# Optimization experiments

Measured on AMD Instinct MI355X. Metric: run time of the kernel, lower is better.

Reference implementation:

```python
import jax, jax.numpy as jnp
import numpy as np

DIM = 768
HEADS = 12
CLS = 20
HIDDEN = 4 * DIM
EPS = 1e-5


def layernorm(x, g, b):
    m = jnp.mean(x, axis=-1, keepdims=True)
    v = jnp.var(x, axis=-1, keepdims=True)
    return (x - m) * jax.lax.rsqrt(v + EPS) * g + b


def setup_inputs() -> dict:
    key = jax.random.key(0)
    ks = jax.random.split(key, 8)
    s = 0.02
    return {
        "x": jax.random.normal(ks[0], (16, 596, DIM), dtype=jnp.float32),
        "qkv_w": jax.random.normal(ks[1], (3 * DIM, DIM), dtype=jnp.float32) * s,
        "qkv_b": jnp.zeros((3 * DIM,), jnp.float32),
        "proj_w": jax.random.normal(ks[2], (DIM, DIM), dtype=jnp.float32) * s,
        "proj_b": jnp.zeros((DIM,), jnp.float32),
        "ln1_g": jnp.ones((DIM,), jnp.float32),
        "ln1_b": jnp.zeros((DIM,), jnp.float32),
        "ln2_g": jnp.ones((DIM,), jnp.float32),
        "ln2_b": jnp.zeros((DIM,), jnp.float32),
        "fc1_w": jax.random.normal(ks[3], (HIDDEN, DIM), dtype=jnp.float32) * s,
        "fc1_b": jnp.zeros((HIDDEN,), jnp.float32),
        "fc2_w": jax.random.normal(ks[4], (DIM, HIDDEN), dtype=jnp.float32) * s,
        "fc2_b": jnp.zeros((DIM,), jnp.float32),
    }


def attention(x, qkv_w, qkv_b, proj_w, proj_b):
    B, N, C = x.shape
    hd = C // HEADS
    scale = hd ** -0.5
    qkv = x @ qkv_w.T + qkv_b  # [B,N,3C]
    qkv = qkv.reshape(B, N, 3, HEADS, hd).transpose(2, 0, 3, 1, 4)
    q, k, v = qkv[0], qkv[1], qkv[2]  # [B,h,N,hd]
    attn = jnp.einsum("bhqd,bhkd->bhqk", q, k) * scale  # [B,h,N,N]
    # split softmax: first CLS key-columns normalized among themselves,
    # remaining patch columns normalized among themselves.
    attn_cls = jax.nn.softmax(attn[..., :CLS], axis=-1)
    attn_pat = jax.nn.softmax(attn[..., CLS:], axis=-1)
    attn = jnp.concatenate([attn_cls, attn_pat], axis=-1)
    weights = attn
    o = jnp.einsum("bhqk,bhkd->bhqd", attn, v)
    o = o.transpose(0, 2, 1, 3).reshape(B, N, C)
    o = o @ proj_w.T + proj_b
    return o, weights


def reference(x, qkv_w, qkv_b, proj_w, proj_b, ln1_g, ln1_b, ln2_g, ln2_b,
              fc1_w, fc1_b, fc2_w, fc2_b):
    o, weights = attention(layernorm(x, ln1_g, ln1_b), qkv_w, qkv_b, proj_w, proj_b)
    x = x + o
    h = layernorm(x, ln2_g, ln2_b)
    h = jax.nn.gelu(h @ fc1_w.T + fc1_b, approximate=False)
    h = h @ fc2_w.T + fc2_b
    x = x + h
    return x, weights
```

## Files before the change

kernel.cpp:

```cpp
#include <hip/hip_runtime.h>
#include <math.h>

constexpr int DIMC   = 768;
constexpr int NHEADS = 12;
constexpr int HD     = 64;
constexpr int NCLS   = 20;
constexpr int HID    = 3072;
constexpr int NBATCH = 16;
constexpr int NSEQ   = 596;
constexpr int NT     = NBATCH * NSEQ;
constexpr int C3     = 3 * DIMC;
constexpr int MH     = NT / 2;
#define LN_EPS 1e-5f

typedef __attribute__((ext_vector_type(8))) short short8;
typedef __attribute__((ext_vector_type(4))) float f32x4;

__device__ __forceinline__ unsigned short bf16_rn(float f) {
    unsigned u = __float_as_uint(f);
    u += 0x7fffu + ((u >> 16) & 1u);
    return (unsigned short)(u >> 16);
}
__device__ __forceinline__ float bf16_tof(unsigned short h) {
    return __uint_as_float(((unsigned)h) << 16);
}

__device__ __forceinline__ float gelu_f(float v) {
    return 0.5f * v * (1.0f + erff(v * 0.70710678118654752f));
}

typedef __attribute__((address_space(1))) const unsigned int gu32;
typedef __attribute__((address_space(3))) unsigned int lu32;
#define GLOAD16(gp, lp) __builtin_amdgcn_global_load_lds((gu32*)(gp), (lu32*)(lp), 16, 0, 0)

__global__ __launch_bounds__(256) void split_kernel(const float* __restrict__ in,
                                                    unsigned short* __restrict__ hi,
                                                    unsigned short* __restrict__ lo,
                                                    int n4) {
    int i = blockIdx.x * 256 + threadIdx.x;
    const int stp = gridDim.x * 256;
    for (; i < n4; i += stp) {
        const float4 v = ((const float4*)in)[i];
        ushort4 h, l;
        h.x = bf16_rn(v.x); l.x = bf16_rn(v.x - bf16_tof(h.x));
        h.y = bf16_rn(v.y); l.y = bf16_rn(v.y - bf16_tof(h.y));
        h.z = bf16_rn(v.z); l.z = bf16_rn(v.z - bf16_tof(h.z));
        h.w = bf16_rn(v.w); l.w = bf16_rn(v.w - bf16_tof(h.w));
        ((ushort4*)hi)[i] = h;
        ((ushort4*)lo)[i] = l;
    }
}

__global__ __launch_bounds__(256) void ln_kernel(const float* __restrict__ x,
                                                 const float* __restrict__ g,
                                                 const float* __restrict__ b,
                                                 unsigned short* __restrict__ yh,
                                                 unsigned short* __restrict__ yl) {
    const int row = blockIdx.x;
    const float* xr = x + (size_t)row * DIMC;
    const int t = threadIdx.x;
    float v0 = xr[t];
    float v1 = xr[t + 256];
    float v2 = xr[t + 512];
    float s  = v0 + v1 + v2;
    float ss = v0 * v0 + v1 * v1 + v2 * v2;
#pragma unroll
    for (int m = 1; m < 64; m <<= 1) {
        s  += __shfl_xor(s, m);
        ss += __shfl_xor(ss, m);
    }
    __shared__ float ls[4], lss[4];
    const int wid = t >> 6;
    if ((t & 63) == 0) { ls[wid] = s; lss[wid] = ss; }
    __syncthreads();
    s  = ls[0] + ls[1] + ls[2] + ls[3];
    ss = lss[0] + lss[1] + lss[2] + lss[3];
    const float mean = s * (1.0f / DIMC);
    const float var  = ss * (1.0f / DIMC) - mean * mean;
    const float rstd = rsqrtf(var + LN_EPS);
    const size_t base = (size_t)row * DIMC;
#pragma unroll
    for (int e = 0; e < 3; e++) {
        const int c = t + e * 256;
        const float v = (e == 0) ? v0 : (e == 1) ? v1 : v2;
        const float y = (v - mean) * rstd * g[c] + b[c];
        const unsigned short h = bf16_rn(y);
        yh[base + c] = h;
        yl[base + c] = bf16_rn(y - bf16_tof(h));
    }
}

template <int EPI>
__global__ __launch_bounds__(256) void mgemm_kernel(
    const unsigned short* __restrict__ Ah, const unsigned short* __restrict__ Al,
    const unsigned short* __restrict__ Wh, const unsigned short* __restrict__ Wl,
    const float* __restrict__ bias, const float* __restrict__ res,
    float* __restrict__ Out, unsigned short* __restrict__ OutH,
    unsigned short* __restrict__ OutL, int M, int N, int K)
{
    __shared__ unsigned short sAh[128 * 64], sAl[128 * 64];
    __shared__ unsigned short sWh[128 * 64], sWl[128 * 64];

    const int tid  = threadIdx.x;
    const int lane = tid & 63, wid = tid >> 6;
    const int m0 = blockIdx.y * 128, n0 = blockIdx.x * 128;
    const int wr = wid >> 1, wc = wid & 1;

    const int sr = lane >> 3;
    const int sg = (lane & 7) ^ sr;
    size_t goffA[4], goffW[4];
    int ldsoff[4];
#pragma unroll
    for (int t = 0; t < 4; t++) {
        const int r = wid * 32 + t * 8 + sr;
        goffA[t] = (size_t)(m0 + r) * K + sg * 8;
        goffW[t] = (size_t)(n0 + r) * K + sg * 8;
        ldsoff[t] = (wid * 4 + t) * 512;
    }

    const int fr = lane & 15, fe = lane >> 4;
    int offA[2][4], offW[2][4];
#pragma unroll
    for (int k32 = 0; k32 < 2; k32++)
#pragma unroll
        for (int i = 0; i < 4; i++) {
            const int cs = ((k32 * 4 + fe) ^ (fr & 7)) * 8;
            offA[k32][i] = (wr * 64 + i * 16 + fr) * 64 + cs;
            offW[k32][i] = (wc * 64 + i * 16 + fr) * 64 + cs;
        }

    f32x4 acc[4][4];
#pragma unroll
    for (int i = 0; i < 4; i++)
#pragma unroll
        for (int j = 0; j < 4; j++) acc[i][j] = {0.f, 0.f, 0.f, 0.f};

#pragma unroll
    for (int t = 0; t < 4; t++) {
        GLOAD16(Ah + goffA[t], &sAh[ldsoff[t]]);
        GLOAD16(Al + goffA[t], &sAl[ldsoff[t]]);
        GLOAD16(Wh + goffW[t], &sWh[ldsoff[t]]);
        GLOAD16(Wl + goffW[t], &sWl[ldsoff[t]]);
    }

    for (int kt = 0; kt < K; kt += 64) {
        __syncthreads();
#pragma unroll
        for (int k32 = 0; k32 < 2; k32++) {
            short8 a_h[4], a_l[4], w_h[4], w_l[4];
#pragma unroll
            for (int i = 0; i < 4; i++) {
                a_h[i] = *(const short8*)&sAh[offA[k32][i]];
                a_l[i] = *(const short8*)&sAl[offA[k32][i]];
                w_h[i] = *(const short8*)&sWh[offW[k32][i]];
                w_l[i] = *(const short8*)&sWl[offW[k32][i]];
            }
#pragma unroll
            for (int i = 0; i < 4; i++)
#pragma unroll
                for (int j = 0; j < 4; j++) {
                    acc[i][j] = __builtin_amdgcn_mfma_f32_16x16x32_bf16(a_h[i], w_h[j], acc[i][j], 0, 0, 0);
                    acc[i][j] = __builtin_amdgcn_mfma_f32_16x16x32_bf16(a_l[i], w_h[j], acc[i][j], 0, 0, 0);
                    acc[i][j] = __builtin_amdgcn_mfma_f32_16x16x32_bf16(a_h[i], w_l[j], acc[i][j], 0, 0, 0);
                }
        }
        __syncthreads();
        if (kt + 64 < K) {
            const size_t ka = (size_t)(kt + 64);
#pragma unroll
            for (int t = 0; t < 4; t++) {
                GLOAD16(Ah + goffA[t] + ka, &sAh[ldsoff[t]]);
                GLOAD16(Al + goffA[t] + ka, &sAl[ldsoff[t]]);
                GLOAD16(Wh + goffW[t] + ka, &sWh[ldsoff[t]]);
                GLOAD16(Wl + goffW[t] + ka, &sWl[ldsoff[t]]);
            }
        }
    }

#pragma unroll
    for (int j = 0; j < 4; j++) {
        const int col = n0 + wc * 64 + j * 16 + fr;
        const float bj = bias[col];
#pragma unroll
        for (int i = 0; i < 4; i++) {
            const int row0 = m0 + wr * 64 + i * 16 + fe * 4;
#pragma unroll
            for (int q = 0; q < 4; q++) {
                const int gm = row0 + q;
                if (gm < M) {
                    const size_t idx = (size_t)gm * N + col;
                    float v = acc[i][j][q] + bj;
                    if (EPI == 1) v += res[idx];
                    if (EPI == 2) {
                        v = gelu_f(v);
                        const unsigned short hh = bf16_rn(v);
                        OutH[idx] = hh;
                        OutL[idx] = bf16_rn(v - bf16_tof(hh));
                    } else if (EPI == 3) {
                        const unsigned short hh = bf16_rn(v);
                        OutH[idx] = hh;
                        OutL[idx] = bf16_rn(v - bf16_tof(hh));
                    } else {
                        Out[idx] = v;
                    }
                }
            }
        }
    }
}

__global__ __launch_bounds__(256) void fattn_kernel(
    const unsigned short* __restrict__ gqh, const unsigned short* __restrict__ gql,
    float* __restrict__ wts,
    unsigned short* __restrict__ oh, unsigned short* __restrict__ ol)
{
    __shared__ unsigned short Kh[4096], Kl[4096];
    __shared__ unsigned short Vh[4096], Vl[4096];
    __shared__ float Plds[4][16 * 68];

    const int tid = threadIdx.x;
    const int lane = tid & 63, w = tid >> 6;
    const int fr = lane & 15, fe = lane >> 4;
    const int bh = blockIdx.x;
    const int b = bh / NHEADS, h = bh - b * NHEADS;
    const int q0 = blockIdx.y * 64 + w * 16;
    const size_t tokbase = (size_t)b * NSEQ;
    const size_t hoff = (size_t)h * HD;
    const size_t wbase = (size_t)bh * NSEQ * NSEQ;

    short8 qfh[2], qfl[2];
    {
        const short8 z8 = {0, 0, 0, 0, 0, 0, 0, 0};
        qfh[0] = z8; qfh[1] = z8; qfl[0] = z8; qfl[1] = z8;
        const int qi = q0 + fr;
        if (qi < NSEQ) {
            const size_t base = (tokbase + qi) * C3 + hoff + fe * 8;
            qfh[0] = *(const short8*)(gqh + base);
            qfh[1] = *(const short8*)(gqh + base + 32);
            qfl[0] = *(const short8*)(gql + base);
            qfl[1] = *(const short8*)(gql + base + 32);
        }
    }

    const int srow = lane >> 3;
    const int sc8 = (lane & 7) ^ srow;

    float mc[4], mp[4], lc[4], lp[4];
#pragma unroll
    for (int r = 0; r < 4; r++) { mc[r] = -3e38f; mp[r] = -3e38f; lc[r] = 0.f; lp[r] = 0.f; }

    for (int ch = 0; ch < 10; ch++) {
        __syncthreads();
#pragma unroll
        for (int i = 0; i < 2; i++) {
            const int s = w + i * 4;
            const int key = min(ch * 64 + s * 8 + srow, NSEQ - 1);
            const size_t src = (tokbase + key) * C3 + DIMC + hoff + sc8 * 8;
            GLOAD16(gqh + src, &Kh[s * 512]);
            GLOAD16(gql + src, &Kl[s * 512]);
        }
        __syncthreads();

        f32x4 sc_[4];
#pragma unroll
        for (int t = 0; t < 4; t++) sc_[t] = {0.f, 0.f, 0.f, 0.f};
#pragma unroll
        for (int k32 = 0; k32 < 2; k32++)
#pragma unroll
            for (int t = 0; t < 4; t++) {
                const int pos = (t * 16 + fr) * 64 + ((k32 * 4 + fe) ^ (fr & 7)) * 8;
                const short8 kbh = *(const short8*)&Kh[pos];
                const short8 kbl = *(const short8*)&Kl[pos];
                sc_[t] = __builtin_amdgcn_mfma_f32_16x16x32_bf16(qfh[k32], kbh, sc_[t], 0, 0, 0);
                sc_[t] = __builtin_amdgcn_mfma_f32_16x16x32_bf16(qfl[k32], kbh, sc_[t], 0, 0, 0);
                sc_[t] = __builtin_amdgcn_mfma_f32_16x16x32_bf16(qfh[k32], kbl, sc_[t], 0, 0, 0);
            }

        float sv[4][4];
#pragma unroll
        for (int t = 0; t < 4; t++)
#pragma unroll
            for (int r = 0; r < 4; r++) {
                float v = sc_[t][r] * 0.125f;
                if (ch * 64 + t * 16 + fr >= NSEQ) v = -3e38f;
                sv[t][r] = v;
            }

        if (ch == 0) {
#pragma unroll
            for (int r = 0; r < 4; r++) {
                float xc = -3e38f, xp = -3e38f;
#pragma unroll
                for (int t = 0; t < 4; t++) {
                    const bool cls = (t == 0) || (t == 1 && fr < 4);
                    if (cls) xc = fmaxf(xc, sv[t][r]); else xp = fmaxf(xp, sv[t][r]);
                }
#pragma unroll
                for (int o = 1; o < 16; o <<= 1) {
                    xc = fmaxf(xc, __shfl_xor(xc, o));
                    xp = fmaxf(xp, __shfl_xor(xp, o));
                }
                const float mcn = fmaxf(mc[r], xc), mpn = fmaxf(mp[r], xp);
                float ec = 0.f, ep = 0.f;
#pragma unroll
                for (int t = 0; t < 4; t++) {
                    const bool cls = (t == 0) || (t == 1 && fr < 4);
                    const float e = expf(sv[t][r] - (cls ? mcn : mpn));
                    if (cls) ec += e; else ep += e;
                }
#pragma unroll
                for (int o = 1; o < 16; o <<= 1) {
                    ec += __shfl_xor(ec, o);
                    ep += __shfl_xor(ep, o);
                }
                lc[r] = lc[r] * expf(mc[r] - mcn) + ec;
                lp[r] = lp[r] * expf(mp[r] - mpn) + ep;
                mc[r] = mcn; mp[r] = mpn;
            }
        } else {
#pragma unroll
            for (int r = 0; r < 4; r++) {
                float xp = fmaxf(fmaxf(sv[0][r], sv[1][r]), fmaxf(sv[2][r], sv[3][r]));
#pragma unroll
                for (int o = 1; o < 16; o <<= 1) xp = fmaxf(xp, __shfl_xor(xp, o));
                const float mpn = fmaxf(mp[r], xp);
                float ep = 0.f;
#pragma unroll
                for (int t = 0; t < 4; t++) ep += expf(sv[t][r] - mpn);
#pragma unroll
                for (int o = 1; o < 16; o <<= 1) ep += __shfl_xor(ep, o);
                lp[r] = lp[r] * expf(mp[r] - mpn) + ep;
                mp[r] = mpn;
            }
        }
    }

    float ic[4], ip[4];
#pragma unroll
    for (int r = 0; r < 4; r++) { ic[r] = 1.f / lc[r]; ip[r] = 1.f / lp[r]; }

    f32x4 oacc[4];
#pragma unroll
    for (int dt = 0; dt < 4; dt++) oacc[dt] = {0.f, 0.f, 0.f, 0.f};

    const int dgq = tid & 7;
    const int kp  = tid >> 3;

    for (int ch = 0; ch < 10; ch++) {
        __syncthreads();
#pragma unroll
        for (int i = 0; i < 2; i++) {
            const int s = w + i * 4;
            const int key = min(ch * 64 + s * 8 + srow, NSEQ - 1);
            const size_t src = (tokbase + key) * C3 + DIMC + hoff + sc8 * 8;
            GLOAD16(gqh + src, &Kh[s * 512]);
            GLOAD16(gql + src, &Kl[s * 512]);
        }
        {
            const short8 z8 = {0, 0, 0, 0, 0, 0, 0, 0};
            short8 vah = z8, vAl = z8, vbh = z8, vbl = z8;
            const int keyA = ch * 64 + kp * 2;
            if (keyA < NSEQ) {
                const size_t oA = (tokbase + keyA) * C3 + 2 * DIMC + hoff + dgq * 8;
                vah = *(const short8*)(gqh + oA);
                vAl = *(const short8*)(gql + oA);
            }
            if (keyA + 1 < NSEQ) {
                const size_t oB = (tokbase + keyA + 1) * C3 + 2 * DIMC + hoff + dgq * 8;
                vbh = *(const short8*)(gqh + oB);
                vbl = *(const short8*)(gql + oB);
            }
#pragma unroll
            for (int e = 0; e < 8; e++) {
                const int d = dgq * 8 + e;
                const int col = ((kp >> 2) ^ e ^ dgq) & 7;
                const int wo = d * 32 + col * 4 + (kp & 3);
                ((unsigned int*)Vh)[wo] =
                    (unsigned int)(unsigned short)vah[e] | ((unsigned int)(unsigned short)vbh[e] << 16);
                ((unsigned int*)Vl)[wo] =
                    (unsigned int)(unsigned short)vAl[e] | ((unsigned int)(unsigned short)vbl[e] << 16);
            }
        }
        __syncthreads();

        f32x4 sc_[4];
#pragma unroll
        for (int t = 0; t < 4; t++) sc_[t] = {0.f, 0.f, 0.f, 0.f};
#pragma unroll
        for (int k32 = 0; k32 < 2; k32++)
#pragma unroll
            for (int t = 0; t < 4; t++) {
                const int pos = (t * 16 + fr) * 64 + ((k32 * 4 + fe) ^ (fr & 7)) * 8;
                const short8 kbh = *(const short8*)&Kh[pos];
                const short8 kbl = *(const short8*)&Kl[pos];
                sc_[t] = __builtin_amdgcn_mfma_f32_16x16x32_bf16(qfh[k32], kbh, sc_[t], 0, 0, 0);
                sc_[t] = __builtin_amdgcn_mfma_f32_16x16x32_bf16(qfl[k32], kbh, sc_[t], 0, 0, 0);
                sc_[t] = __builtin_amdgcn_mfma_f32_16x16x32_bf16(qfh[k32], kbl, sc_[t], 0, 0, 0);
            }

#pragma unroll
        for (int t = 0; t < 4; t++)
#pragma unroll
            for (int r = 0; r < 4; r++) {
                const int key = ch * 64 + t * 16 + fr;
                float v = sc_[t][r] * 0.125f;
                if (key >= NSEQ) v = -3e38f;
                const bool cls = key < NCLS;
                const float wv = expf(v - (cls ? mc[r] : mp[r])) * (cls ? ic[r] : ip[r]);
                const int q = q0 + fe * 4 + r;
                if (q < NSEQ && key < NSEQ)
                    wts[wbase + (size_t)q * NSEQ + key] = wv;
                Plds[w][(fe * 4 + r) * 68 + t * 16 + fr] = wv;
            }

#pragma unroll
        for (int kh2 = 0; kh2 < 2; kh2++) {
            float pv[8];
            *(float4*)&pv[0] = *(const float4*)&Plds[w][fr * 68 + kh2 * 32 + fe * 8];
            *(float4*)&pv[4] = *(const float4*)&Plds[w][fr * 68 + kh2 * 32 + fe * 8 + 4];
            short8 ph, pl;
#pragma unroll
            for (int j = 0; j < 8; j++) {
                const unsigned short hh = bf16_rn(pv[j]);
                ph[j] = (short)hh;
                pl[j] = (short)bf16_rn(pv[j] - bf16_tof(hh));
            }
#pragma unroll
            for (int dt = 0; dt < 4; dt++) {
                const int d = dt * 16 + fr;
                const int col = ((kh2 * 4 + fe) ^ (d & 7) ^ ((d >> 3) & 7)) & 7;
                const short8 vfh = *(const short8*)&Vh[d * 64 + col * 8];
                const short8 vfl = *(const short8*)&Vl[d * 64 + col * 8];
                oacc[dt] = __builtin_amdgcn_mfma_f32_16x16x32_bf16(ph, vfh, oacc[dt], 0, 0, 0);
                oacc[dt] = __builtin_amdgcn_mfma_f32_16x16x32_bf16(pl, vfh, oacc[dt], 0, 0, 0);
                oacc[dt] = __builtin_amdgcn_mfma_f32_16x16x32_bf16(ph, vfl, oacc[dt], 0, 0, 0);
            }
        }
    }

#pragma unroll
    for (int dt = 0; dt < 4; dt++)
#pragma unroll
        for (int r = 0; r < 4; r++) {
            const int q = q0 + fe * 4 + r;
            if (q < NSEQ) {
                const size_t idx = (tokbase + q) * DIMC + hoff + dt * 16 + fr;
                const float v = oacc[dt][r];
                const unsigned short hh = bf16_rn(v);
                oh[idx] = hh;
                ol[idx] = bf16_rn(v - bf16_tof(hh));
            }
        }
}

extern "C" void kernel_launch(void* const* d_in, const int* in_sizes, int n_in,
                              void* d_out, int out_size, void* d_ws, size_t ws_size,
                              hipStream_t stream) {
    const float* x      = (const float*)d_in[0];
    const float* qkv_w  = (const float*)d_in[1];
    const float* qkv_b  = (const float*)d_in[2];
    const float* proj_w = (const float*)d_in[3];
    const float* proj_b = (const float*)d_in[4];
    const float* ln1_g  = (const float*)d_in[5];
    const float* ln1_b  = (const float*)d_in[6];
    const float* ln2_g  = (const float*)d_in[7];
    const float* ln2_b  = (const float*)d_in[8];
    const float* fc1_w  = (const float*)d_in[9];
    const float* fc1_b  = (const float*)d_in[10];
    const float* fc2_w  = (const float*)d_in[11];
    const float* fc2_b  = (const float*)d_in[12];

    float* out0 = (float*)d_out;
    float* wts  = out0 + (size_t)NT * DIMC;

    char* ws = (char*)d_ws;
    unsigned short* qkv_h = (unsigned short*)ws;
    unsigned short* qkv_l = qkv_h + (size_t)NT * C3;
    unsigned short* hh_h = (unsigned short*)ws;
    unsigned short* hh_l = hh_h + (size_t)MH * HID;
    char* sReg = ws + (size_t)NT * C3 * 4;
    unsigned short* s_h = (unsigned short*)sReg;
    unsigned short* s_l = s_h + (size_t)NT * DIMC;
    float* x1 = (float*)(sReg + (size_t)NT * DIMC * 4);
    char* wReg = (char*)x1 + (size_t)NT * DIMC * 4;
    unsigned short* qw_h = (unsigned short*)wReg;
    unsigned short* qw_l = qw_h + (size_t)C3 * DIMC;
    unsigned short* pw_h = qw_l + (size_t)C3 * DIMC;
    unsigned short* pw_l = pw_h + (size_t)DIMC * DIMC;
    unsigned short* f1_h = pw_l + (size_t)DIMC * DIMC;
    unsigned short* f1_l = f1_h + (size_t)HID * DIMC;
    unsigned short* f2_h = f1_l + (size_t)HID * DIMC;
    unsigned short* f2_l = f2_h + (size_t)DIMC * HID;

    ln_kernel<<<NT, 256, 0, stream>>>(x, ln1_g, ln1_b, s_h, s_l);
    split_kernel<<<1024, 256, 0, stream>>>(qkv_w, qw_h, qw_l, C3 * DIMC / 4);
    split_kernel<<<576, 256, 0, stream>>>(proj_w, pw_h, pw_l, DIMC * DIMC / 4);
    split_kernel<<<1024, 256, 0, stream>>>(fc1_w, f1_h, f1_l, HID * DIMC / 4);
    split_kernel<<<1024, 256, 0, stream>>>(fc2_w, f2_h, f2_l, DIMC * HID / 4);
    mgemm_kernel<3><<<dim3(C3 / 128, (NT + 127) / 128), 256, 0, stream>>>(
        s_h, s_l, qw_h, qw_l, qkv_b, nullptr, nullptr, qkv_h, qkv_l, NT, C3, DIMC);
    fattn_kernel<<<dim3(NBATCH * NHEADS, 10), 256, 0, stream>>>(qkv_h, qkv_l, wts, s_h, s_l);
    mgemm_kernel<1><<<dim3(DIMC / 128, (NT + 127) / 128), 256, 0, stream>>>(
        s_h, s_l, pw_h, pw_l, proj_b, x, x1, nullptr, nullptr, NT, DIMC, DIMC);
    ln_kernel<<<NT, 256, 0, stream>>>(x1, ln2_g, ln2_b, s_h, s_l);
    for (int hf = 0; hf < 2; hf++) {
        const size_t r0 = (size_t)hf * MH;
        mgemm_kernel<2><<<dim3(HID / 128, (MH + 127) / 128), 256, 0, stream>>>(
            s_h + r0 * DIMC, s_l + r0 * DIMC, f1_h, f1_l, fc1_b, nullptr,
            nullptr, hh_h, hh_l, MH, HID, DIMC);
        mgemm_kernel<1><<<dim3(DIMC / 128, (MH + 127) / 128), 256, 0, stream>>>(
            hh_h, hh_l, f2_h, f2_l, fc2_b, x1 + r0 * DIMC,
            out0 + r0 * DIMC, nullptr, nullptr, MH, DIMC, HID);
    }
}
```

Baseline: 1.245 ms.

## Double-buffer GEMM LDS tiles with packed hi/lo halves and XCD-aware block swizzle

The split-bf16 GEMM now stages K-tiles of 32 with the hi and lo parts packed into one 64-wide LDS row. It double-buffers them so the next tile's global loads are issued before the current tile's MFMAs, which drops one barrier per step. Launches become 1D, and block IDs are remapped so consecutive tiles land on the same XCD, to improve L2 locality. The attention output also skips the lo-residual rounding when the value is exactly representable in bf16. The cost is more loop iterations with smaller K steps and more complex address math.

```diff
diff --git a/kernel.cpp b/kernel.cpp
--- a/kernel.cpp
+++ b/kernel.cpp
@@ -92,89 +92,91 @@
 
 template <int EPI>
 __global__ __launch_bounds__(256) void mgemm_kernel(
-    const unsigned short* __restrict__ Ah, const unsigned short* __restrict__ Al,
-    const unsigned short* __restrict__ Wh, const unsigned short* __restrict__ Wl,
+    const unsigned short* __restrict__ Ah, const unsigned short* __restrict__ Wh,
+    int AloOff, int WloOff,
     const float* __restrict__ bias, const float* __restrict__ res,
     float* __restrict__ Out, unsigned short* __restrict__ OutH,
     unsigned short* __restrict__ OutL, int M, int N, int K)
 {
-    __shared__ unsigned short sAh[128 * 64], sAl[128 * 64];
-    __shared__ unsigned short sWh[128 * 64], sWl[128 * 64];
+    __shared__ unsigned short S[2][2][128 * 64];
 
     const int tid  = threadIdx.x;
     const int lane = tid & 63, wid = tid >> 6;
-    const int m0 = blockIdx.y * 128, n0 = blockIdx.x * 128;
+
+    const int gx = N >> 7;
+    const int nb = gridDim.x;
+    const int qq = nb >> 3, rr = nb & 7;
+    const int xcd = blockIdx.x & 7, bix = blockIdx.x >> 3;
+    const int swz = (xcd < rr ? xcd * (qq + 1) : rr * (qq + 1) + (xcd - rr) * qq) + bix;
+    const int m0 = (swz / gx) * 128, n0 = (swz % gx) * 128;
     const int wr = wid >> 1, wc = wid & 1;
 
-    const int sr = lane >> 3;
-    const int sg = (lane & 7) ^ sr;
     size_t goffA[4], goffW[4];
     int ldsoff[4];
 #pragma unroll
-    for (int t = 0; t < 4; t++) {
-        const int r = wid * 32 + t * 8 + sr;
-        goffA[t] = (size_t)(m0 + r) * K + sg * 8;
-        goffW[t] = (size_t)(n0 + r) * K + sg * 8;
-        ldsoff[t] = (wid * 4 + t) * 512;
+    for (int i = 0; i < 4; i++) {
+        const int rloc = wid * 32 + i * 8 + (lane >> 3);
+        const int u = (lane & 7) ^ (rloc & 7);
+        const int chunk = u & 3, isLo = u >> 2;
+        goffA[i] = (size_t)(m0 + rloc) * K + chunk * 8 + (isLo ? AloOff : 0);
+        goffW[i] = (size_t)(n0 + rloc) * K + chunk * 8 + (isLo ? WloOff : 0);
+        ldsoff[i] = (wid * 4 + i) * 512;
     }
 
     const int fr = lane & 15, fe = lane >> 4;
-    int offA[2][4], offW[2][4];
-#pragma unroll
-    for (int k32 = 0; k32 < 2; k32++)
+    int offAhi[4], offAlo[4], offWhi[4], offWlo[4];
+#pragma unroll
+    for (int i = 0; i < 4; i++) {
+        const int ra = wr * 64 + i * 16 + fr;
+        const int rw = wc * 64 + i * 16 + fr;
+        offAhi[i] = ra * 64 + (fe ^ (ra & 7)) * 8;
+        offAlo[i] = ra * 64 + ((fe ^ 4) ^ (ra & 7)) * 8;
+        offWhi[i] = rw * 64 + (fe ^ (rw & 7)) * 8;
+        offWlo[i] = rw * 64 + ((fe ^ 4) ^ (rw & 7)) * 8;
+    }
+
+    f32x4 acc[4][4];
+#pragma unroll
+    for (int i = 0; i < 4; i++)
+#pragma unroll
+        for (int j = 0; j < 4; j++) acc[i][j] = {0.f, 0.f, 0.f, 0.f};
+
+    const int nt = K >> 5;
+#pragma unroll
+    for (int i = 0; i < 4; i++) {
+        GLOAD16(Ah + goffA[i], &S[0][0][ldsoff[i]]);
+        GLOAD16(Wh + goffW[i], &S[0][1][ldsoff[i]]);
+    }
+
+    for (int t = 0; t < nt; t++) {
+        __syncthreads();
+        if (t + 1 < nt) {
+            const int nxt = (t + 1) & 1;
+            const size_t ka = (size_t)(t + 1) << 5;
+#pragma unroll
+            for (int i = 0; i < 4; i++) {
+                GLOAD16(Ah + goffA[i] + ka, &S[nxt][0][ldsoff[i]]);
+                GLOAD16(Wh + goffW[i] + ka, &S[nxt][1][ldsoff[i]]);
+            }
+        }
+        const unsigned short* sA = &S[t & 1][0][0];
+        const unsigned short* sW = &S[t & 1][1][0];
+        short8 a_h[4], a_l[4], w_h[4], w_l[4];
 #pragma unroll
         for (int i = 0; i < 4; i++) {
-            const int cs = ((k32 * 4 + fe) ^ (fr & 7)) * 8;
-            offA[k32][i] = (wr * 64 + i * 16 + fr) * 64 + cs;
-            offW[k32][i] = (wc * 64 + i * 16 + fr) * 64 + cs;
-        }
-
-    f32x4 acc[4][4];
-#pragma unroll
-    for (int i = 0; i < 4; i++)
-#pragma unroll
-        for (int j = 0; j < 4; j++) acc[i][j] = {0.f, 0.f, 0.f, 0.f};
-
-#pragma unroll
-    for (int t = 0; t < 4; t++) {
-        GLOAD16(Ah + goffA[t], &sAh[ldsoff[t]]);
-        GLOAD16(Al + goffA[t], &sAl[ldsoff[t]]);
-        GLOAD16(Wh + goffW[t], &sWh[ldsoff[t]]);
-        GLOAD16(Wl + goffW[t], &sWl[ldsoff[t]]);
-    }
-
-    for (int kt = 0; kt < K; kt += 64) {
-        __syncthreads();
-#pragma unroll
-        for (int k32 = 0; k32 < 2; k32++) {
-            short8 a_h[4], a_l[4], w_h[4], w_l[4];
-#pragma unroll
-            for (int i = 0; i < 4; i++) {
-                a_h[i] = *(const short8*)&sAh[offA[k32][i]];
-                a_l[i] = *(const short8*)&sAl[offA[k32][i]];
-                w_h[i] = *(const short8*)&sWh[offW[k32][i]];
-                w_l[i] = *(const short8*)&sWl[offW[k32][i]];
-            }
-#pragma unroll
-            for (int i = 0; i < 4; i++)
-#pragma unroll
-                for (int j = 0; j < 4; j++) {
-                    acc[i][j] = __builtin_amdgcn_mfma_f32_16x16x32_bf16(a_h[i], w_h[j], acc[i][j], 0, 0, 0);
-                    acc[i][j] = __builtin_amdgcn_mfma_f32_16x16x32_bf16(a_l[i], w_h[j], acc[i][j], 0, 0, 0);
-                    acc[i][j] = __builtin_amdgcn_mfma_f32_16x16x32_bf16(a_h[i], w_l[j], acc[i][j], 0, 0, 0);
-                }
-        }
-        __syncthreads();
-        if (kt + 64 < K) {
-            const size_t ka = (size_t)(kt + 64);
-#pragma unroll
-            for (int t = 0; t < 4; t++) {
-                GLOAD16(Ah + goffA[t] + ka, &sAh[ldsoff[t]]);
-                GLOAD16(Al + goffA[t] + ka, &sAl[ldsoff[t]]);
-                GLOAD16(Wh + goffW[t] + ka, &sWh[ldsoff[t]]);
-                GLOAD16(Wl + goffW[t] + ka, &sWl[ldsoff[t]]);
-            }
-        }
+            a_h[i] = *(const short8*)&sA[offAhi[i]];
+            a_l[i] = *(const short8*)&sA[offAlo[i]];
+            w_h[i] = *(const short8*)&sW[offWhi[i]];
+            w_l[i] = *(const short8*)&sW[offWlo[i]];
+        }
+#pragma unroll
+        for (int i = 0; i < 4; i++)
+#pragma unroll
+            for (int j = 0; j < 4; j++) {
+                acc[i][j] = __builtin_amdgcn_mfma_f32_16x16x32_bf16(a_h[i], w_h[j], acc[i][j], 0, 0, 0);
+                acc[i][j] = __builtin_amdgcn_mfma_f32_16x16x32_bf16(a_l[i], w_h[j], acc[i][j], 0, 0, 0);
+                acc[i][j] = __builtin_amdgcn_mfma_f32_16x16x32_bf16(a_h[i], w_l[j], acc[i][j], 0, 0, 0);
+            }
     }
 
 #pragma unroll
@@ -448,7 +450,7 @@
                 const float v = oacc[dt][r];
                 const unsigned short hh = bf16_rn(v);
                 oh[idx] = hh;
-                ol[idx] = bf16_rn(v - bf16_tof(hh));
+                ol[idx] = bf16_tof(hh) == v ? 0 : bf16_rn(v - bf16_tof(hh));
             }
         }
 }
@@ -497,19 +499,21 @@
     split_kernel<<<576, 256, 0, stream>>>(proj_w, pw_h, pw_l, DIMC * DIMC / 4);
     split_kernel<<<1024, 256, 0, stream>>>(fc1_w, f1_h, f1_l, HID * DIMC / 4);
     split_kernel<<<1024, 256, 0, stream>>>(fc2_w, f2_h, f2_l, DIMC * HID / 4);
-    mgemm_kernel<3><<<dim3(C3 / 128, (NT + 127) / 128), 256, 0, stream>>>(
-        s_h, s_l, qw_h, qw_l, qkv_b, nullptr, nullptr, qkv_h, qkv_l, NT, C3, DIMC);
+    mgemm_kernel<3><<<(C3 / 128) * ((NT + 127) / 128), 256, 0, stream>>>(
+        s_h, qw_h, NT * DIMC, C3 * DIMC, qkv_b, nullptr,
+        nullptr, qkv_h, qkv_l, NT, C3, DIMC);
     fattn_kernel<<<dim3(NBATCH * NHEADS, 10), 256, 0, stream>>>(qkv_h, qkv_l, wts, s_h, s_l);
-    mgemm_kernel<1><<<dim3(DIMC / 128, (NT + 127) / 128), 256, 0, stream>>>(
-        s_h, s_l, pw_h, pw_l, proj_b, x, x1, nullptr, nullptr, NT, DIMC, DIMC);
+    mgemm_kernel<1><<<(DIMC / 128) * ((NT + 127) / 128), 256, 0, stream>>>(
+        s_h, pw_h, NT * DIMC, DIMC * DIMC, proj_b, x,
+        x1, nullptr, nullptr, NT, DIMC, DIMC);
     ln_kernel<<<NT, 256, 0, stream>>>(x1, ln2_g, ln2_b, s_h, s_l);
     for (int hf = 0; hf < 2; hf++) {
         const size_t r0 = (size_t)hf * MH;
-        mgemm_kernel<2><<<dim3(HID / 128, (MH + 127) / 128), 256, 0, stream>>>(
-            s_h + r0 * DIMC, s_l + r0 * DIMC, f1_h, f1_l, fc1_b, nullptr,
+        mgemm_kernel<2><<<(HID / 128) * ((MH + 127) / 128), 256, 0, stream>>>(
+            s_h + r0 * DIMC, f1_h, NT * DIMC, HID * DIMC, fc1_b, nullptr,
             nullptr, hh_h, hh_l, MH, HID, DIMC);
-        mgemm_kernel<1><<<dim3(DIMC / 128, (MH + 127) / 128), 256, 0, stream>>>(
-            hh_h, hh_l, f2_h, f2_l, fc2_b, x1 + r0 * DIMC,
+        mgemm_kernel<1><<<(DIMC / 128) * ((MH + 127) / 128), 256, 0, stream>>>(
+            hh_h, f2_h, MH * HID, DIMC * HID, fc2_b, x1 + r0 * DIMC,
             out0 + r0 * DIMC, nullptr, nullptr, MH, DIMC, HID);
     }
 }
```

New measurement: 1.192 ms. 1.04x faster.
